# Kernel tuning notes

Measured on AMD Instinct MI355X. Metric: run time of the kernel, lower is better.

Reference implementation:

```python
import jax, jax.numpy as jnp
import numpy as np

B, S, E, H, D = 4, 2048, 1024, 16, 64  # batch, seq, embed, heads, head_dim


def setup_inputs() -> dict:
    key = jax.random.key(0)
    k1, k2, k3 = jax.random.split(key, 3)
    x = jax.random.normal(k1, (B, S, E), dtype=jnp.float32)
    qkv_w = jax.random.normal(k2, (E, H, 3 * D), dtype=jnp.float32) * (1.0 / np.sqrt(E))
    qkv_b = jnp.zeros((H, 3 * D), dtype=jnp.float32)
    out_w = jax.random.normal(k3, (H, D, E), dtype=jnp.float32) * (1.0 / np.sqrt(H * D))
    out_b = jnp.zeros((E,), dtype=jnp.float32)
    return {"x": x, "qkv_w": qkv_w, "qkv_b": qkv_b, "out_w": out_w, "out_b": out_b}


def _large_negative_number(dtype):
    return jnp.asarray(-0.7 * jnp.finfo(dtype).max, dtype=dtype)


def reference(x, qkv_w, qkv_b, out_w, out_b):
    # qkv projection: LinearGeneral(E -> (H, 3D))
    qkv = jnp.einsum('bse,ehd->bshd', x, qkv_w) + qkv_b  # [B,S,H,3D]
    q, k, v = jnp.split(qkv, 3, axis=-1)  # each [B,S,H,D]
    logits = jnp.einsum('bqhd,bkhd->bhqk', q, k)  # [B,H,S,S]
    logits = logits / jnp.sqrt(jnp.asarray(q.shape[-1], logits.dtype))
    mask = jnp.tril(jnp.ones((q.shape[1], q.shape[1]), dtype=jnp.bool_))
    logits = jnp.where(mask, logits, _large_negative_number(logits.dtype))
    probs = jax.nn.softmax(logits, axis=-1)
    attn = jnp.einsum('bhqk,bkhd->bqhd', probs, v)  # [B,S,H,D]
    # output projection: LinearGeneral((H, D) -> E)
    return jnp.einsum('bqhd,hde->bqe', attn, out_w) + out_b
```

## Files before the change

### kernel.cpp

```cpp
#include <hip/hip_runtime.h>

typedef unsigned int u32;
typedef _Float16 f16;
typedef _Float16 f16x8 __attribute__((ext_vector_type(8)));
typedef _Float16 f16x4 __attribute__((ext_vector_type(4)));
typedef float f32x4 __attribute__((ext_vector_type(4)));

#define LOG2E 1.4426950408889634f

__device__ __forceinline__ void gl_lds16(const void* g, void* l) {
  __builtin_amdgcn_global_load_lds(
      (const __attribute__((address_space(1))) u32*)g,
      (__attribute__((address_space(3))) u32*)l, 16, 0, 0);
}

__device__ __forceinline__ f32x4 mfma16(f16x8 a, f16x8 b, f32x4 c) {
  return __builtin_amdgcn_mfma_f32_16x16x32_f16(a, b, c, 0, 0, 0);
}

__global__ void k_cvt(const float* __restrict__ in, f16* __restrict__ out, int n4) {
  int stride = gridDim.x * blockDim.x;
  for (int i = blockIdx.x * blockDim.x + threadIdx.x; i < n4; i += stride) {
    f32x4 v = *(const f32x4*)(in + (size_t)i * 4);
    f16x4 o;
    o[0] = (f16)v[0]; o[1] = (f16)v[1]; o[2] = (f16)v[2]; o[3] = (f16)v[3];
    *(f16x4*)(out + (size_t)i * 4) = o;
  }
}

__global__ void k_tconv(const float* __restrict__ in, f16* __restrict__ out, int R, int C) {
  __shared__ f16 tile[32][33];
  int c0 = blockIdx.x * 32, r0 = blockIdx.y * 32;
  int tx = threadIdx.x, ty = threadIdx.y;
#pragma unroll
  for (int i = ty; i < 32; i += 8)
    tile[i][tx] = (f16)in[(size_t)(r0 + i) * C + c0 + tx];
  __syncthreads();
#pragma unroll
  for (int i = ty; i < 32; i += 8)
    out[(size_t)(c0 + i) * R + r0 + tx] = tile[tx][i];
}

__global__ __launch_bounds__(256) void k_gemm_qkv(
    const f16* __restrict__ A, const f16* __restrict__ Bt,
    const float* __restrict__ bias,
    f16* __restrict__ qo, f16* __restrict__ ko2, f16* __restrict__ vto) {
  constexpr int K = 1024;
  __shared__ __align__(16) f16 As[128 * 32];
  __shared__ __align__(16) f16 Bs[128 * 32];
  const int bn = blockIdx.x * 128, bm = blockIdx.y * 128;
  const int t = threadIdx.x, lane = t & 63, w = t >> 6;
  const int wr = w >> 1, wc = w & 1;
  const int g = lane >> 4, rl = lane & 15;

  const int c0 = t, c1 = 256 + t;
  const int r0 = c0 >> 2, s0 = (c0 & 3) ^ ((r0 >> 1) & 3);
  const int r1 = c1 >> 2, s1 = (c1 & 3) ^ ((r1 >> 1) & 3);
  const f16* a0 = A + (size_t)(bm + r0) * K + s0 * 8;
  const f16* a1 = A + (size_t)(bm + r1) * K + s1 * 8;
  const f16* b0 = Bt + (size_t)(bn + r0) * K + s0 * 8;
  const f16* b1 = Bt + (size_t)(bn + r1) * K + s1 * 8;
  f16* lA0 = As + w * 512;
  f16* lA1 = As + 2048 + w * 512;
  f16* lB0 = Bs + w * 512;
  f16* lB1 = Bs + 2048 + w * 512;

  f32x4 acc[4][4] = {};

  for (int kt = 0; kt < K / 32; ++kt) {
    const int kof = kt * 32;
    gl_lds16(a0 + kof, lA0);
    gl_lds16(a1 + kof, lA1);
    gl_lds16(b0 + kof, lB0);
    gl_lds16(b1 + kof, lB1);
    __syncthreads();
    f16x8 af[4], bfr[4];
#pragma unroll
    for (int i = 0; i < 4; ++i) {
      int row = wr * 64 + i * 16 + rl;
      af[i] = *(const f16x8*)(As + row * 32 + ((g ^ ((row >> 1) & 3)) * 8));
      int col = wc * 64 + i * 16 + rl;
      bfr[i] = *(const f16x8*)(Bs + col * 32 + ((g ^ ((col >> 1) & 3)) * 8));
    }
#pragma unroll
    for (int i = 0; i < 4; ++i)
#pragma unroll
      for (int j = 0; j < 4; ++j)
        acc[i][j] = mfma16(af[i], bfr[j], acc[i][j]);
    __syncthreads();
  }

#pragma unroll
  for (int i = 0; i < 4; ++i)
#pragma unroll
    for (int j = 0; j < 4; ++j)
#pragma unroll
      for (int r = 0; r < 4; ++r) {
        int m = bm + wr * 64 + i * 16 + g * 4 + r;
        int n = bn + wc * 64 + j * 16 + rl;
        float v = acc[i][j][r] + bias[n];
        int b = m >> 11, s = m & 2047;
        int h = n / 192, rem = n - h * 192;
        int tsel = rem >> 6, d = rem & 63;
        size_t bh = (size_t)(b * 16 + h);
        if (tsel == 0)      qo[(bh * 2048 + s) * 64 + d] = (f16)(v * (0.125f * LOG2E));
        else if (tsel == 1) ko2[(bh * 2048 + s) * 64 + d] = (f16)v;
        else                vto[(bh * 64 + d) * 2048 + s] = (f16)v;
      }
}

__global__ __launch_bounds__(256, 4) void k_attn2(
    const f16* __restrict__ q, const f16* __restrict__ kgl,
    const f16* __restrict__ vt, f16* __restrict__ o) {
  constexpr int S = 2048;
  __shared__ __align__(16) f16 Ks[2][64 * 64];
  __shared__ __align__(16) f16 Vs[2][64 * 64];
  __shared__ __align__(16) f16 Ps[4][16 * 64];

  const int blk = blockIdx.x;
  const int sidx = blk >> 3;
  const int bh = (blk & 7) * 8 + (sidx & 7);
  const int qb = 15 - (sidx >> 3);

  const int t = threadIdx.x, lane = t & 63, w = t >> 6;
  const int g = lane >> 4, rl = lane & 15;

  const f16* qp = q + ((size_t)bh * S + qb * 128) * 64;
  const f16* kb = kgl + (size_t)bh * S * 64;
  const f16* vb = vt + (size_t)bh * 64 * S;

  f16x8 qf[2][2];
#pragma unroll
  for (int sub = 0; sub < 2; ++sub)
#pragma unroll
    for (int ks = 0; ks < 2; ++ks)
      qf[sub][ks] = *(const f16x8*)(qp + (size_t)(w * 32 + sub * 16 + rl) * 64 + ks * 32 + g * 8);

  f32x4 oacc[2][4] = {};
  float lrow[2] = {0.f, 0.f};

  const int srow = lane >> 3;
  const int sslot = (lane & 7) ^ srow;

  const int nkt = 2 * qb + 2;
  const int qmaxw = qb * 128 + w * 32 + 31;

  auto STAGE = [&](int bufi, int kt) {
#pragma unroll
    for (int i = 0; i < 2; ++i) {
      const int r0 = w * 16 + i * 8;
      gl_lds16(kb + (size_t)(kt * 64 + r0 + srow) * 64 + sslot * 8, &Ks[bufi][r0 * 64]);
      gl_lds16(vb + (size_t)(r0 + srow) * S + kt * 64 + sslot * 8, &Vs[bufi][r0 * 64]);
    }
  };

  STAGE(0, 0);
  __syncthreads();
  int buf = 0;

  for (int kt = 0; kt < nkt; ++kt) {
    if (kt + 1 < nkt) STAGE(buf ^ 1, kt + 1);

    if (kt * 64 <= qmaxw) {
      const f16* Kb = &Ks[buf][0];
      const f16* Vb = &Vs[buf][0];
#pragma unroll
      for (int sub = 0; sub < 2; ++sub) {
        const int qsub = qb * 128 + w * 32 + sub * 16;
        if (kt * 64 > qsub + 15) continue;

        f32x4 sT[4] = {};
#pragma unroll
        for (int j = 0; j < 4; ++j)
#pragma unroll
          for (int ks = 0; ks < 2; ++ks) {
            int row = j * 16 + rl;
            f16x8 kf = *(const f16x8*)(Kb + row * 64 + (((ks * 4 + g) ^ (rl & 7)) * 8));
            sT[j] = mfma16(kf, qf[sub][ks], sT[j]);
          }

        if (kt * 64 + 63 > qsub) {
#pragma unroll
          for (int j = 0; j < 4; ++j)
#pragma unroll
            for (int r = 0; r < 4; ++r)
              if (kt * 64 + j * 16 + g * 4 + r > qsub + rl) sT[j][r] = -1e30f;
        }

        float ps = 0.f;
#pragma unroll
        for (int j = 0; j < 4; ++j) {
          f16x4 pb;
#pragma unroll
          for (int r = 0; r < 4; ++r) {
            float p = exp2f(sT[j][r]);
            ps += p;
            pb[r] = (f16)p;
          }
          *(f16x4*)(&Ps[w][0] + rl * 64 + (((j * 2 + (g >> 1)) ^ (rl & 7)) * 8) + (g & 1) * 4) = pb;
        }
        lrow[sub] += ps;

        asm volatile("s_waitcnt lgkmcnt(0)" ::: "memory");
        __builtin_amdgcn_sched_barrier(0);

        f16x8 pf[2];
#pragma unroll
        for (int ks = 0; ks < 2; ++ks)
          pf[ks] = *(const f16x8*)(&Ps[w][0] + rl * 64 + (((ks * 4 + g) ^ (rl & 7)) * 8));

#pragma unroll
        for (int dj = 0; dj < 4; ++dj)
#pragma unroll
          for (int ks = 0; ks < 2; ++ks) {
            int vrow = dj * 16 + rl;
            f16x8 vf = *(const f16x8*)(Vb + vrow * 64 + (((ks * 4 + g) ^ (rl & 7)) * 8));
            oacc[sub][dj] = mfma16(pf[ks], vf, oacc[sub][dj]);
          }
      }
    }
    __syncthreads();
    buf ^= 1;
  }

  float rinv[2];
#pragma unroll
  for (int sub = 0; sub < 2; ++sub) {
    float s_ = lrow[sub];
    s_ += __shfl_xor(s_, 16, 64);
    s_ += __shfl_xor(s_, 32, 64);
    rinv[sub] = 1.0f / s_;
  }

  const int h = bh & 15;
  const size_t rowb = (size_t)(bh >> 4) * 2048 + qb * 128 + w * 32;
#pragma unroll
  for (int sub = 0; sub < 2; ++sub)
#pragma unroll
    for (int r = 0; r < 4; ++r) {
      float ri = __shfl(rinv[sub], g * 4 + r, 64);
#pragma unroll
      for (int dj = 0; dj < 4; ++dj)
        o[(rowb + sub * 16 + g * 4 + r) * 1024 + h * 64 + dj * 16 + rl] =
            (f16)(oacc[sub][dj][r] * ri);
    }
}

__global__ __launch_bounds__(256) void k_gemm_out(
    const f16* __restrict__ A, const f16* __restrict__ Bt,
    const float* __restrict__ bias, float* __restrict__ out) {
  constexpr int K = 1024;
  __shared__ __align__(16) f16 As[128 * 32];
  __shared__ __align__(16) f16 Bs[128 * 32];
  const int bn = blockIdx.x * 128, bm = blockIdx.y * 128;
  const int t = threadIdx.x, lane = t & 63, w = t >> 6;
  const int wr = w >> 1, wc = w & 1;
  const int g = lane >> 4, rl = lane & 15;

  const int c0 = t, c1 = 256 + t;
  const int r0 = c0 >> 2, s0 = (c0 & 3) ^ ((r0 >> 1) & 3);
  const int r1 = c1 >> 2, s1 = (c1 & 3) ^ ((r1 >> 1) & 3);
  const f16* a0 = A + (size_t)(bm + r0) * K + s0 * 8;
  const f16* a1 = A + (size_t)(bm + r1) * K + s1 * 8;
  const f16* b0 = Bt + (size_t)(bn + r0) * K + s0 * 8;
  const f16* b1 = Bt + (size_t)(bn + r1) * K + s1 * 8;
  f16* lA0 = As + w * 512;
  f16* lA1 = As + 2048 + w * 512;
  f16* lB0 = Bs + w * 512;
  f16* lB1 = Bs + 2048 + w * 512;

  f32x4 acc[4][4] = {};

  for (int kt = 0; kt < K / 32; ++kt) {
    const int kof = kt * 32;
    gl_lds16(a0 + kof, lA0);
    gl_lds16(a1 + kof, lA1);
    gl_lds16(b0 + kof, lB0);
    gl_lds16(b1 + kof, lB1);
    __syncthreads();
    f16x8 af[4], bfr[4];
#pragma unroll
    for (int i = 0; i < 4; ++i) {
      int row = wr * 64 + i * 16 + rl;
      af[i] = *(const f16x8*)(As + row * 32 + ((g ^ ((row >> 1) & 3)) * 8));
      int col = wc * 64 + i * 16 + rl;
      bfr[i] = *(const f16x8*)(Bs + col * 32 + ((g ^ ((col >> 1) & 3)) * 8));
    }
#pragma unroll
    for (int i = 0; i < 4; ++i)
#pragma unroll
      for (int j = 0; j < 4; ++j)
        acc[i][j] = mfma16(af[i], bfr[j], acc[i][j]);
    __syncthreads();
  }

#pragma unroll
  for (int i = 0; i < 4; ++i)
#pragma unroll
    for (int j = 0; j < 4; ++j)
#pragma unroll
      for (int r = 0; r < 4; ++r) {
        int m = bm + wr * 64 + i * 16 + g * 4 + r;
        int n = bn + wc * 64 + j * 16 + rl;
        out[(size_t)m * 1024 + n] = acc[i][j][r] + bias[n];
      }
}

extern "C" void kernel_launch(void* const* d_in, const int* in_sizes, int n_in,
                              void* d_out, int out_size, void* d_ws, size_t ws_size,
                              hipStream_t stream) {
  (void)in_sizes; (void)n_in; (void)out_size; (void)ws_size;
  const float* x    = (const float*)d_in[0];
  const float* wqkv = (const float*)d_in[1];
  const float* bqkv = (const float*)d_in[2];
  const float* wo   = (const float*)d_in[3];
  const float* bo   = (const float*)d_in[4];
  float* out = (float*)d_out;
  char* ws = (char*)d_ws;

  f16* xb    = (f16*)(ws + 0);
  f16* wqkvt = (f16*)(ws + 16777216);
  f16* wot   = (f16*)(ws + 23068672);
  f16* qws   = (f16*)(ws + 25165824);
  f16* kws   = (f16*)(ws + 41943040);
  f16* vtws  = (f16*)(ws + 58720256);
  f16* attnb = xb;

  k_cvt<<<2048, 256, 0, stream>>>(x, xb, 8388608 / 4);
  k_tconv<<<dim3(96, 32), dim3(32, 8), 0, stream>>>(wqkv, wqkvt, 1024, 3072);
  k_tconv<<<dim3(32, 32), dim3(32, 8), 0, stream>>>(wo, wot, 1024, 1024);
  k_gemm_qkv<<<dim3(24, 64), 256, 0, stream>>>(xb, wqkvt, bqkv, qws, kws, vtws);
  k_attn2<<<1024, 256, 0, stream>>>(qws, kws, vtws, attnb);
  k_gemm_out<<<dim3(8, 64), 256, 0, stream>>>(attnb, wot, bo, out);
}
```

Measured before the change: 197.8 us.

## Double-buffer GEMM staging, remap block order, batch attention QK MFMAs, widen conversion

Both GEMMs now share one helper that stages the next K tile into a second shared-memory buffer while computing on the current one. It raises MFMA priority with setprio and remaps block IDs into groups of eight for L2 locality. The attention kernel computes QK scores for both 16-row subtiles in one interleaved MFMA loop, reusing each K fragment. It also reorders query-block scheduling to balance causal work across the launch. The fp32-to-fp16 conversion kernel now processes eight elements per thread. Doubling shared memory and the occupancy hint of 3 may reduce concurrent blocks, and the fused QK loop raises register pressure.

```diff
diff --git a/kernel.cpp b/kernel.cpp
--- a/kernel.cpp
+++ b/kernel.cpp
@@ -18,13 +18,15 @@
   return __builtin_amdgcn_mfma_f32_16x16x32_f16(a, b, c, 0, 0, 0);
 }
 
-__global__ void k_cvt(const float* __restrict__ in, f16* __restrict__ out, int n4) {
+__global__ void k_cvt(const float* __restrict__ in, f16* __restrict__ out, int n8) {
   int stride = gridDim.x * blockDim.x;
-  for (int i = blockIdx.x * blockDim.x + threadIdx.x; i < n4; i += stride) {
-    f32x4 v = *(const f32x4*)(in + (size_t)i * 4);
-    f16x4 o;
-    o[0] = (f16)v[0]; o[1] = (f16)v[1]; o[2] = (f16)v[2]; o[3] = (f16)v[3];
-    *(f16x4*)(out + (size_t)i * 4) = o;
+  for (int i = blockIdx.x * blockDim.x + threadIdx.x; i < n8; i += stride) {
+    f32x4 a = *(const f32x4*)(in + (size_t)i * 8);
+    f32x4 b = *(const f32x4*)(in + (size_t)i * 8 + 4);
+    f16x8 o;
+    o[0] = (f16)a[0]; o[1] = (f16)a[1]; o[2] = (f16)a[2]; o[3] = (f16)a[3];
+    o[4] = (f16)b[0]; o[5] = (f16)b[1]; o[6] = (f16)b[2]; o[7] = (f16)b[3];
+    *(f16x8*)(out + (size_t)i * 8) = o;
   }
 }
 
@@ -41,54 +43,67 @@
     out[(size_t)(c0 + i) * R + r0 + tx] = tile[tx][i];
 }
 
-__global__ __launch_bounds__(256) void k_gemm_qkv(
+__device__ __forceinline__ void gemm97(
+    const f16* __restrict__ A, const f16* __restrict__ Bt,
+    int bm, int bn, f16* SM, int w, int lane, f32x4 (&acc)[4][4]) {
+  constexpr int KT = 32;
+  const int g = lane >> 4, rl = lane & 15;
+  const int l4 = lane >> 2, ls = lane & 3;
+  const int sslot = ls ^ ((l4 >> 1) & 3);
+  const int wr = w >> 1, wc = w & 1;
+
+  const f16* aS = A + (size_t)(bm + w * 16 + l4) * 1024 + sslot * 8;
+  const f16* bS = Bt + (size_t)(bn + w * 16 + l4) * 1024 + sslot * 8;
+
+#define STG97(b, kt) do { \
+    gl_lds16(aS + (kt) * 32,          SM + (b) * 8192 + w * 512); \
+    gl_lds16(aS + 65536 + (kt) * 32,  SM + (b) * 8192 + 2048 + w * 512); \
+    gl_lds16(bS + (kt) * 32,          SM + (b) * 8192 + 4096 + w * 512); \
+    gl_lds16(bS + 65536 + (kt) * 32,  SM + (b) * 8192 + 6144 + w * 512); } while (0)
+
+  const int ro = rl * 32 + ((g ^ ((rl >> 1) & 3)) * 8);
+
+  STG97(0, 0);
+  __syncthreads();
+
+#pragma unroll 1
+  for (int kt = 0; kt < KT; ++kt) {
+    const int cur = kt & 1;
+    if (kt + 1 < KT) STG97(cur ^ 1, kt + 1);
+    const f16* SMb = SM + cur * 8192;
+    f16x8 af[4], bf[4];
+#pragma unroll
+    for (int mi = 0; mi < 4; ++mi)
+      af[mi] = *(const f16x8*)(SMb + wr * 2048 + mi * 512 + ro);
+#pragma unroll
+    for (int j = 0; j < 4; ++j)
+      bf[j] = *(const f16x8*)(SMb + 4096 + wc * 2048 + j * 512 + ro);
+    __builtin_amdgcn_s_setprio(1);
+#pragma unroll
+    for (int mi = 0; mi < 4; ++mi)
+#pragma unroll
+      for (int j = 0; j < 4; ++j)
+        acc[mi][j] = mfma16(af[mi], bf[j], acc[mi][j]);
+    __builtin_amdgcn_s_setprio(0);
+    __syncthreads();
+  }
+#undef STG97
+}
+
+__global__ __launch_bounds__(256, 3) void k_gemm_qkv5(
     const f16* __restrict__ A, const f16* __restrict__ Bt,
     const float* __restrict__ bias,
     f16* __restrict__ qo, f16* __restrict__ ko2, f16* __restrict__ vto) {
-  constexpr int K = 1024;
-  __shared__ __align__(16) f16 As[128 * 32];
-  __shared__ __align__(16) f16 Bs[128 * 32];
-  const int bn = blockIdx.x * 128, bm = blockIdx.y * 128;
+  __shared__ __align__(16) f16 SM[16384];
+  const int lin0 = blockIdx.y * 24 + blockIdx.x;
+  const int lin = (lin0 & 7) * 192 + (lin0 >> 3);
+  const int bn = (lin % 24) * 128, bm = (lin / 24) * 128;
   const int t = threadIdx.x, lane = t & 63, w = t >> 6;
+  const int g = lane >> 4, rl = lane & 15;
   const int wr = w >> 1, wc = w & 1;
-  const int g = lane >> 4, rl = lane & 15;
-
-  const int c0 = t, c1 = 256 + t;
-  const int r0 = c0 >> 2, s0 = (c0 & 3) ^ ((r0 >> 1) & 3);
-  const int r1 = c1 >> 2, s1 = (c1 & 3) ^ ((r1 >> 1) & 3);
-  const f16* a0 = A + (size_t)(bm + r0) * K + s0 * 8;
-  const f16* a1 = A + (size_t)(bm + r1) * K + s1 * 8;
-  const f16* b0 = Bt + (size_t)(bn + r0) * K + s0 * 8;
-  const f16* b1 = Bt + (size_t)(bn + r1) * K + s1 * 8;
-  f16* lA0 = As + w * 512;
-  f16* lA1 = As + 2048 + w * 512;
-  f16* lB0 = Bs + w * 512;
-  f16* lB1 = Bs + 2048 + w * 512;
 
   f32x4 acc[4][4] = {};
-
-  for (int kt = 0; kt < K / 32; ++kt) {
-    const int kof = kt * 32;
-    gl_lds16(a0 + kof, lA0);
-    gl_lds16(a1 + kof, lA1);
-    gl_lds16(b0 + kof, lB0);
-    gl_lds16(b1 + kof, lB1);
-    __syncthreads();
-    f16x8 af[4], bfr[4];
-#pragma unroll
-    for (int i = 0; i < 4; ++i) {
-      int row = wr * 64 + i * 16 + rl;
-      af[i] = *(const f16x8*)(As + row * 32 + ((g ^ ((row >> 1) & 3)) * 8));
-      int col = wc * 64 + i * 16 + rl;
-      bfr[i] = *(const f16x8*)(Bs + col * 32 + ((g ^ ((col >> 1) & 3)) * 8));
-    }
-#pragma unroll
-    for (int i = 0; i < 4; ++i)
-#pragma unroll
-      for (int j = 0; j < 4; ++j)
-        acc[i][j] = mfma16(af[i], bfr[j], acc[i][j]);
-    __syncthreads();
-  }
+  gemm97(A, Bt, bm, bn, SM, w, lane, acc);
 
 #pragma unroll
   for (int i = 0; i < 4; ++i)
@@ -101,15 +116,41 @@
         float v = acc[i][j][r] + bias[n];
         int b = m >> 11, s = m & 2047;
         int h = n / 192, rem = n - h * 192;
-        int tsel = rem >> 6, d = rem & 63;
+        int tsel = rem >> 6, dd = rem & 63;
         size_t bh = (size_t)(b * 16 + h);
-        if (tsel == 0)      qo[(bh * 2048 + s) * 64 + d] = (f16)(v * (0.125f * LOG2E));
-        else if (tsel == 1) ko2[(bh * 2048 + s) * 64 + d] = (f16)v;
-        else                vto[(bh * 64 + d) * 2048 + s] = (f16)v;
+        if (tsel == 0)      qo[(bh * 2048 + s) * 64 + dd] = (f16)(v * (0.125f * LOG2E));
+        else if (tsel == 1) ko2[(bh * 2048 + s) * 64 + dd] = (f16)v;
+        else                vto[(bh * 64 + dd) * 2048 + s] = (f16)v;
       }
 }
 
-__global__ __launch_bounds__(256, 4) void k_attn2(
+__global__ __launch_bounds__(256, 3) void k_gemm_out5(
+    const f16* __restrict__ A, const f16* __restrict__ Bt,
+    const float* __restrict__ bias, float* __restrict__ out) {
+  __shared__ __align__(16) f16 SM[16384];
+  const int lin0 = blockIdx.y * 8 + blockIdx.x;
+  const int lin = (lin0 & 7) * 64 + (lin0 >> 3);
+  const int bn = (lin % 8) * 128, bm = (lin / 8) * 128;
+  const int t = threadIdx.x, lane = t & 63, w = t >> 6;
+  const int g = lane >> 4, rl = lane & 15;
+  const int wr = w >> 1, wc = w & 1;
+
+  f32x4 acc[4][4] = {};
+  gemm97(A, Bt, bm, bn, SM, w, lane, acc);
+
+#pragma unroll
+  for (int i = 0; i < 4; ++i)
+#pragma unroll
+    for (int j = 0; j < 4; ++j)
+#pragma unroll
+      for (int r = 0; r < 4; ++r) {
+        int m = bm + wr * 64 + i * 16 + g * 4 + r;
+        int n = bn + wc * 64 + j * 16 + rl;
+        out[(size_t)m * 1024 + n] = acc[i][j][r] + bias[n];
+      }
+}
+
+__global__ __launch_bounds__(256, 4) void k_attn5(
     const f16* __restrict__ q, const f16* __restrict__ kgl,
     const f16* __restrict__ vt, f16* __restrict__ o) {
   constexpr int S = 2048;
@@ -117,10 +158,10 @@
   __shared__ __align__(16) f16 Vs[2][64 * 64];
   __shared__ __align__(16) f16 Ps[4][16 * 64];
 
-  const int blk = blockIdx.x;
-  const int sidx = blk >> 3;
-  const int bh = (blk & 7) * 8 + (sidx & 7);
-  const int qb = 15 - (sidx >> 3);
+  const int d = blockIdx.x;
+  const int bh = (d & 7) * 8 + ((d >> 3) & 7);
+  const int v_ = d >> 6, g2 = v_ >> 2, r2 = v_ & 3;
+  const int qb = (g2 == 0) ? 15 - r2 : (g2 == 1) ? r2 : (g2 == 2) ? 11 - r2 : 4 + r2;
 
   const int t = threadIdx.x, lane = t & 63, w = t >> 6;
   const int g = lane >> 4, rl = lane & 15;
@@ -143,7 +184,8 @@
   const int sslot = (lane & 7) ^ srow;
 
   const int nkt = 2 * qb + 2;
-  const int qmaxw = qb * 128 + w * 32 + 31;
+  const int qsub0 = qb * 128 + w * 32;
+  const int qmaxw = qsub0 + 31;
 
   auto STAGE = [&](int bufi, int kt) {
 #pragma unroll
@@ -164,28 +206,34 @@
     if (kt * 64 <= qmaxw) {
       const f16* Kb = &Ks[buf][0];
       const f16* Vb = &Vs[buf][0];
+
+      f32x4 sT[2][4] = {};
+#pragma unroll
+      for (int j = 0; j < 4; ++j)
+#pragma unroll
+        for (int ks = 0; ks < 2; ++ks) {
+          int row = j * 16 + rl;
+          f16x8 kf = *(const f16x8*)(Kb + row * 64 + (((ks * 4 + g) ^ (rl & 7)) * 8));
+          sT[0][j] = mfma16(kf, qf[0][ks], sT[0][j]);
+          sT[1][j] = mfma16(kf, qf[1][ks], sT[1][j]);
+        }
+
+      if (kt * 64 + 63 > qsub0) {
+#pragma unroll
+        for (int sub = 0; sub < 2; ++sub) {
+          const int qs = qsub0 + sub * 16;
+#pragma unroll
+          for (int j = 0; j < 4; ++j)
+#pragma unroll
+            for (int r = 0; r < 4; ++r)
+              if (kt * 64 + j * 16 + g * 4 + r > qs + rl) sT[sub][j][r] = -1e30f;
+        }
+      }
+
 #pragma unroll
       for (int sub = 0; sub < 2; ++sub) {
-        const int qsub = qb * 128 + w * 32 + sub * 16;
+        const int qsub = qsub0 + sub * 16;
         if (kt * 64 > qsub + 15) continue;
-
-        f32x4 sT[4] = {};
-#pragma unroll
-        for (int j = 0; j < 4; ++j)
-#pragma unroll
-          for (int ks = 0; ks < 2; ++ks) {
-            int row = j * 16 + rl;
-            f16x8 kf = *(const f16x8*)(Kb + row * 64 + (((ks * 4 + g) ^ (rl & 7)) * 8));
-            sT[j] = mfma16(kf, qf[sub][ks], sT[j]);
-          }
-
-        if (kt * 64 + 63 > qsub) {
-#pragma unroll
-          for (int j = 0; j < 4; ++j)
-#pragma unroll
-            for (int r = 0; r < 4; ++r)
-              if (kt * 64 + j * 16 + g * 4 + r > qsub + rl) sT[j][r] = -1e30f;
-        }
 
         float ps = 0.f;
 #pragma unroll
@@ -193,9 +241,9 @@
           f16x4 pb;
 #pragma unroll
           for (int r = 0; r < 4; ++r) {
-            float p = exp2f(sT[j][r]);
-            ps += p;
-            pb[r] = (f16)p;
+            float pp = exp2f(sT[sub][j][r]);
+            ps += pp;
+            pb[r] = (f16)pp;
           }
           *(f16x4*)(&Ps[w][0] + rl * 64 + (((j * 2 + (g >> 1)) ^ (rl & 7)) * 8) + (g & 1) * 4) = pb;
         }
@@ -244,66 +292,6 @@
         o[(rowb + sub * 16 + g * 4 + r) * 1024 + h * 64 + dj * 16 + rl] =
             (f16)(oacc[sub][dj][r] * ri);
     }
-}
-
-__global__ __launch_bounds__(256) void k_gemm_out(
-    const f16* __restrict__ A, const f16* __restrict__ Bt,
-    const float* __restrict__ bias, float* __restrict__ out) {
-  constexpr int K = 1024;
-  __shared__ __align__(16) f16 As[128 * 32];
-  __shared__ __align__(16) f16 Bs[128 * 32];
-  const int bn = blockIdx.x * 128, bm = blockIdx.y * 128;
-  const int t = threadIdx.x, lane = t & 63, w = t >> 6;
-  const int wr = w >> 1, wc = w & 1;
-  const int g = lane >> 4, rl = lane & 15;
-
-  const int c0 = t, c1 = 256 + t;
-  const int r0 = c0 >> 2, s0 = (c0 & 3) ^ ((r0 >> 1) & 3);
-  const int r1 = c1 >> 2, s1 = (c1 & 3) ^ ((r1 >> 1) & 3);
-  const f16* a0 = A + (size_t)(bm + r0) * K + s0 * 8;
-  const f16* a1 = A + (size_t)(bm + r1) * K + s1 * 8;
-  const f16* b0 = Bt + (size_t)(bn + r0) * K + s0 * 8;
-  const f16* b1 = Bt + (size_t)(bn + r1) * K + s1 * 8;
-  f16* lA0 = As + w * 512;
-  f16* lA1 = As + 2048 + w * 512;
-  f16* lB0 = Bs + w * 512;
-  f16* lB1 = Bs + 2048 + w * 512;
-
-  f32x4 acc[4][4] = {};
-
-  for (int kt = 0; kt < K / 32; ++kt) {
-    const int kof = kt * 32;
-    gl_lds16(a0 + kof, lA0);
-    gl_lds16(a1 + kof, lA1);
-    gl_lds16(b0 + kof, lB0);
-    gl_lds16(b1 + kof, lB1);
-    __syncthreads();
-    f16x8 af[4], bfr[4];
-#pragma unroll
-    for (int i = 0; i < 4; ++i) {
-      int row = wr * 64 + i * 16 + rl;
-      af[i] = *(const f16x8*)(As + row * 32 + ((g ^ ((row >> 1) & 3)) * 8));
-      int col = wc * 64 + i * 16 + rl;
-      bfr[i] = *(const f16x8*)(Bs + col * 32 + ((g ^ ((col >> 1) & 3)) * 8));
-    }
-#pragma unroll
-    for (int i = 0; i < 4; ++i)
-#pragma unroll
-      for (int j = 0; j < 4; ++j)
-        acc[i][j] = mfma16(af[i], bfr[j], acc[i][j]);
-    __syncthreads();
-  }
-
-#pragma unroll
-  for (int i = 0; i < 4; ++i)
-#pragma unroll
-    for (int j = 0; j < 4; ++j)
-#pragma unroll
-      for (int r = 0; r < 4; ++r) {
-        int m = bm + wr * 64 + i * 16 + g * 4 + r;
-        int n = bn + wc * 64 + j * 16 + rl;
-        out[(size_t)m * 1024 + n] = acc[i][j][r] + bias[n];
-      }
 }
 
 extern "C" void kernel_launch(void* const* d_in, const int* in_sizes, int n_in,
@@ -326,10 +314,10 @@
   f16* vtws  = (f16*)(ws + 58720256);
   f16* attnb = xb;
 
-  k_cvt<<<2048, 256, 0, stream>>>(x, xb, 8388608 / 4);
+  k_cvt<<<1024, 256, 0, stream>>>(x, xb, 8388608 / 8);
   k_tconv<<<dim3(96, 32), dim3(32, 8), 0, stream>>>(wqkv, wqkvt, 1024, 3072);
   k_tconv<<<dim3(32, 32), dim3(32, 8), 0, stream>>>(wo, wot, 1024, 1024);
-  k_gemm_qkv<<<dim3(24, 64), 256, 0, stream>>>(xb, wqkvt, bqkv, qws, kws, vtws);
-  k_attn2<<<1024, 256, 0, stream>>>(qws, kws, vtws, attnb);
-  k_gemm_out<<<dim3(8, 64), 256, 0, stream>>>(attnb, wot, bo, out);
-}
+  k_gemm_qkv5<<<dim3(24, 64), 256, 0, stream>>>(xb, wqkvt, bqkv, qws, kws, vtws);
+  k_attn5<<<1024, 256, 0, stream>>>(qws, kws, vtws, attnb);
+  k_gemm_out5<<<dim3(8, 64), 256, 0, stream>>>(attnb, wot, bo, out);
+}
```

Result: faster. 187.0 us (-5.5%).
